# Kernel tuning notes

Hardware: AMD Instinct MI355X
Metric: run time of the kernel (lower is better)

## Reference

```python
import jax, jax.numpy as jnp
import numpy as np

DIM = 256
NUM_HEADS = 4
WINDOW = 64
EPS = 1e-6


def setup_inputs() -> dict:
    key = jax.random.key(0)
    ks = jax.random.split(key, 12)
    d = DIM
    s = 0.02
    return {
        "x": jax.random.normal(ks[0], (4, 2049, d), dtype=jnp.float32),
        "norm1_w": jnp.ones((d,), jnp.float32),
        "in_proj_w": jax.random.normal(ks[1], (3 * d, d), jnp.float32) * s,
        "in_proj_b": jnp.zeros((3 * d,), jnp.float32),
        "out_proj_w": jax.random.normal(ks[2], (d, d), jnp.float32) * s,
        "out_proj_b": jnp.zeros((d,), jnp.float32),
        "norm2_w": jnp.ones((d,), jnp.float32),
        "w1": jax.random.normal(ks[3], (2 * d, d), jnp.float32) * s,
        "b1": jnp.zeros((2 * d,), jnp.float32),
        "w2": jax.random.normal(ks[4], (d, 2 * d), jnp.float32) * s,
        "b2": jnp.zeros((d,), jnp.float32),
    }


def _rmsnorm(x, w):
    r = jax.lax.rsqrt(jnp.mean(x * x, axis=-1, keepdims=True) + EPS)
    return x * r * w


def _factorized_mask(size):
    # global token 0 attends/attended everywhere; others banded within WINDOW
    idx = jnp.arange(size)
    band = jnp.abs(idx[:, None] - idx[None, :]) <= WINDOW
    allowed = band | (idx[:, None] == 0) | (idx[None, :] == 0)
    return jnp.where(allowed, 0.0, -jnp.inf).astype(jnp.float32)


def reference(x, norm1_w, in_proj_w, in_proj_b, out_proj_w, out_proj_b,
              norm2_w, w1, b1, w2, b2):
    B, S, D = x.shape
    H = NUM_HEADS
    dh = D // H
    residual = x
    h = _rmsnorm(x, norm1_w)
    # fused qkv projection (torch MHA in_proj): [B,S,3D]
    qkv = h @ in_proj_w.T + in_proj_b
    q, k, v = jnp.split(qkv, 3, axis=-1)
    q = q.reshape(B, S, H, dh).transpose(0, 2, 1, 3)  # [B,H,S,dh]
    k = k.reshape(B, S, H, dh).transpose(0, 2, 1, 3)
    v = v.reshape(B, S, H, dh).transpose(0, 2, 1, 3)
    scores = jnp.einsum("bhqd,bhkd->bhqk", q, k) / jnp.sqrt(jnp.float32(dh))
    scores = scores + _factorized_mask(S)  # additive -inf mask
    attn = jax.nn.softmax(scores, axis=-1)
    ctx = jnp.einsum("bhqk,bhkd->bhqd", attn, v)
    ctx = ctx.transpose(0, 2, 1, 3).reshape(B, S, D)
    attn_out = ctx @ out_proj_w.T + out_proj_b
    x1 = residual + attn_out
    h2 = _rmsnorm(x1, norm2_w)
    ffn = jax.nn.gelu(h2 @ w1.T + b1, approximate=False) @ w2.T + b2
    return x1 + ffn
```

## Files before the change

kernel.cpp:

```cpp
#include <hip/hip_runtime.h>
#include <hip/hip_bf16.h>
#include <math.h>

#define BATCH 4
#define SEQ 2049
#define DIMD 256
#define WIN 64
#define M_ROWS (BATCH * SEQ)
#define M_PAD 8320

#define QT16 129
#define NKB 10
#define PSTR 168
#define CSTR 264
#define GSTR 136
#define VGUARD 64
#define VW 2256
#define QKSTR 512

#define NSPLIT 33
#define VT_F4 288768

typedef __attribute__((ext_vector_type(8))) short short8;
typedef __attribute__((ext_vector_type(4))) float f32x4;
typedef __hip_bfloat16 bf16;

__device__ __forceinline__ float b2f(short u) {
    union { unsigned int i; float f; } c;
    c.i = ((unsigned int)(unsigned short)u) << 16;
    return c.f;
}
__device__ __forceinline__ short f2b(float f) {
    bf16 h = __float2bfloat16(f);
    return *reinterpret_cast<short*>(&h);
}

__global__ __launch_bounds__(256) void prep_kernel(
        const float* __restrict__ wq, const float* __restrict__ wo,
        const float* __restrict__ w1, const float* __restrict__ w2,
        bf16* __restrict__ oq, bf16* __restrict__ oo,
        bf16* __restrict__ o1, bf16* __restrict__ o2,
        const float* __restrict__ x, const float* __restrict__ nw,
        bf16* __restrict__ h, float4* __restrict__ vTz) {
    const int bi = blockIdx.x, tid = threadIdx.x;
    if (bi < 2048) {
        int i = bi * 256 + tid;
        if (i < 196608)      oq[i]          = __float2bfloat16(wq[i]);
        else if (i < 262144) oo[i - 196608] = __float2bfloat16(wo[i - 196608]);
        else if (i < 393216) o1[i - 262144] = __float2bfloat16(w1[i - 262144]);
        else                 o2[i - 393216] = __float2bfloat16(w2[i - 393216]);
        return;
    }
    if (bi >= 4097) {
        int zi = (bi - 4097) * 256 + tid;
        #pragma unroll
        for (int it = 0; it < 3; it++) {
            int idx = zi + it * 512 * 256;
            if (idx < VT_F4) vTz[idx] = (float4){0.f, 0.f, 0.f, 0.f};
        }
        return;
    }
    int wid = tid >> 6, lane = tid & 63;
    int row = (bi - 2048) * 4 + wid;
    if (row >= M_ROWS) return;
    const float4 v = reinterpret_cast<const float4*>(x + (size_t)row * DIMD)[lane];
    float ss = v.x * v.x + v.y * v.y + v.z * v.z + v.w * v.w;
    #pragma unroll
    for (int o = 1; o < 64; o <<= 1) ss += __shfl_xor(ss, o, 64);
    float r = rsqrtf(ss * (1.0f / DIMD) + 1e-6f);
    const float4 wv = reinterpret_cast<const float4*>(nw)[lane];
    bf16* hp = h + (size_t)row * DIMD + lane * 4;
    hp[0] = __float2bfloat16(v.x * r * wv.x);
    hp[1] = __float2bfloat16(v.y * r * wv.y);
    hp[2] = __float2bfloat16(v.z * r * wv.z);
    hp[3] = __float2bfloat16(v.w * r * wv.w);
}

__global__ __launch_bounds__(256) void gemm_qkv(
        const bf16* __restrict__ A, const bf16* __restrict__ B,
        const float* __restrict__ bias, bf16* __restrict__ qk, short* __restrict__ vT) {
    __shared__ __align__(16) short lA[8 * 128 * 8];
    __shared__ __align__(16) short lB[8 * 128 * 8];
    const int tid = threadIdx.x, lane = tid & 63, wid = tid >> 6;
    const int m0 = blockIdx.x * 128;
    const int n0 = blockIdx.y * 128;
    const int wr = wid >> 1, wc = wid & 1;
    const int r = lane & 15, g = lane >> 4;
    const int K = 256;

    f32x4 acc[4][4];
    #pragma unroll
    for (int i = 0; i < 4; i++)
        #pragma unroll
        for (int j = 0; j < 4; j++) acc[i][j] = (f32x4){0.f, 0.f, 0.f, 0.f};

    for (int k0 = 0; k0 < K; k0 += 64) {
        #pragma unroll
        for (int it = 0; it < 4; ++it) {
            int c = it * 256 + tid;
            int kc = c >> 7, row = c & 127;
            __builtin_amdgcn_global_load_lds(
                (const __attribute__((address_space(1))) void*)(A + (size_t)(m0 + row) * K + k0 + kc * 8),
                (__attribute__((address_space(3))) void*)&lA[c * 8], 16, 0, 0);
        }
        #pragma unroll
        for (int it = 0; it < 4; ++it) {
            int c = it * 256 + tid;
            int kc = c >> 7, row = c & 127;
            __builtin_amdgcn_global_load_lds(
                (const __attribute__((address_space(1))) void*)(B + (size_t)(n0 + row) * K + k0 + kc * 8),
                (__attribute__((address_space(3))) void*)&lB[c * 8], 16, 0, 0);
        }
        __syncthreads();
        #pragma unroll
        for (int kk = 0; kk < 2; kk++) {
            short8 a[4], b[4];
            #pragma unroll
            for (int mi = 0; mi < 4; mi++)
                a[mi] = *reinterpret_cast<const short8*>(&lA[((kk * 4 + g) * 128 + wr * 64 + mi * 16 + r) * 8]);
            #pragma unroll
            for (int ni = 0; ni < 4; ni++)
                b[ni] = *reinterpret_cast<const short8*>(&lB[((kk * 4 + g) * 128 + wc * 64 + ni * 16 + r) * 8]);
            #pragma unroll
            for (int mi = 0; mi < 4; mi++)
                #pragma unroll
                for (int ni = 0; ni < 4; ni++)
                    acc[mi][ni] = __builtin_amdgcn_mfma_f32_16x16x32_bf16(a[mi], b[ni], acc[mi][ni], 0, 0, 0);
        }
        __syncthreads();
    }

    const int c0 = lane & 15, r0 = (lane >> 4) * 4;
    const bool isV = (n0 >= 512);
    #pragma unroll
    for (int mi = 0; mi < 4; mi++) {
        #pragma unroll
        for (int ni = 0; ni < 4; ni++) {
            int col = n0 + wc * 64 + ni * 16 + c0;
            float bv = bias[col];
            #pragma unroll
            for (int j = 0; j < 4; j++) {
                int row = m0 + wr * 64 + mi * 16 + r0 + j;
                if (row < M_ROWS) {
                    float v = acc[mi][ni][j] + bv;
                    if (!isV) {
                        qk[(size_t)row * QKSTR + col] = __float2bfloat16(v);
                    } else {
                        int dcol = col - 512, hh = dcol >> 6, d = dcol & 63;
                        int bb = row >> 11;
                        int js = row - bb * SEQ;
                        if (js < 0) { bb--; js += SEQ; }
                        vT[((size_t)((bb * 4 + hh) * 64 + d)) * VW + VGUARD + js] = f2b(v);
                    }
                }
            }
        }
    }
}

__global__ __launch_bounds__(256) void attn_partial(const bf16* __restrict__ qk,
                                                    const short* __restrict__ vT,
                                                    float* __restrict__ part) {
    __shared__ float q_s[64];
    __shared__ float p_s[64];
    __shared__ float meta[2];
    __shared__ float osum[4][64];
    const int tid = threadIdx.x;
    const int bh = blockIdx.x / NSPLIT, s = blockIdx.x % NSPLIT;
    const int b = bh >> 2, h = bh & 3;
    const size_t base = (size_t)b * SEQ;
    const int j0 = s * 64;
    const int lane = tid & 63, wid = tid >> 6;

    if (tid < 64) q_s[tid] = __bfloat162float(qk[base * QKSTR + h * 64 + tid]);
    __syncthreads();

    if (wid == 0) {
        int j = j0 + lane;
        float sc = -1e30f;
        if (j < SEQ) {
            const short8* kp = reinterpret_cast<const short8*>(
                reinterpret_cast<const short*>(qk) + (base + j) * QKSTR + 256 + h * 64);
            float acc = 0.f;
            #pragma unroll
            for (int d8 = 0; d8 < 8; ++d8) {
                short8 kv = kp[d8];
                #pragma unroll
                for (int e = 0; e < 8; ++e) acc += q_s[d8 * 8 + e] * b2f(kv[e]);
            }
            sc = acc * 0.125f;
        }
        float mx = sc;
        #pragma unroll
        for (int o = 1; o < 64; o <<= 1) mx = fmaxf(mx, __shfl_xor(mx, o, 64));
        float p = (j < SEQ) ? expf(sc - mx) : 0.f;
        p_s[lane] = p;
        float l = p;
        #pragma unroll
        for (int o = 1; o < 64; o <<= 1) l += __shfl_xor(l, o, 64);
        if (lane == 0) { meta[0] = mx; meta[1] = l; }
    }
    __syncthreads();

    const short* vrow = vT + ((size_t)bh * 64 + lane) * VW + VGUARD + j0;
    float oa = 0.f;
    #pragma unroll
    for (int i0 = 0; i0 < 16; i0++) {
        int i = wid + i0 * 4;
        if (j0 + i < SEQ) oa += p_s[i] * b2f(vrow[i]);
    }
    osum[wid][lane] = oa;
    __syncthreads();
    if (wid == 0) {
        float o = osum[0][lane] + osum[1][lane] + osum[2][lane] + osum[3][lane];
        float* pp = part + (size_t)(bh * NSPLIT + s) * 66;
        pp[lane] = o;
        if (lane == 0) { pp[64] = meta[0]; pp[65] = meta[1]; }
    }
}

__global__ __launch_bounds__(256) void attn_or(
        const bf16* __restrict__ qkb, const short* __restrict__ vT,
        const float* __restrict__ part, const bf16* __restrict__ wo,
        const float* __restrict__ ob, const float* __restrict__ x,
        const float* __restrict__ nw, float* __restrict__ x1, bf16* __restrict__ h2) {
    __shared__ short p_lds[4][16][PSTR];
    __shared__ short ctx_lds[16][CSTR];
    __shared__ float osq[4][16];
    const short* qk = reinterpret_cast<const short*>(qkb);
    const int tid = threadIdx.x, lane = tid & 63, h = tid >> 6;
    const int qt = blockIdx.x % QT16;
    const int b = blockIdx.x / QT16;
    const int bh = b * 4 + h;
    const size_t rbase = (size_t)b * SEQ;
    const int q0 = qt * 16;
    const int jbase = q0 - 64;
    const int lrow = lane & 15;
    const int koff = (lane >> 4) * 8;
    const int c0 = lrow, r0 = (lane >> 4) * 4;

    int qrow = q0 + lrow; if (qrow > SEQ - 1) qrow = SEQ - 1;
    const short* qp = qk + (rbase + qrow) * QKSTR + h * 64;
    short8 aq0 = *reinterpret_cast<const short8*>(qp + koff);
    short8 aq1 = *reinterpret_cast<const short8*>(qp + 32 + koff);

    const short* k0p = qk + rbase * QKSTR + 256 + h * 64;
    short8 k0a = *reinterpret_cast<const short8*>(k0p + koff);
    short8 k0b = *reinterpret_cast<const short8*>(k0p + 32 + koff);
    float s0 = 0.f;
    #pragma unroll
    for (int e = 0; e < 8; e++)
        s0 += b2f(aq0[e]) * b2f(k0a[e]) + b2f(aq1[e]) * b2f(k0b[e]);
    s0 += __shfl_xor(s0, 16, 64);
    s0 += __shfl_xor(s0, 32, 64);

    f32x4 s[NKB];
    #pragma unroll
    for (int n = 0; n < NKB; n++) {
        int j = jbase + n * 16 + lrow;
        int jc = j < 0 ? 0 : (j > SEQ - 1 ? SEQ - 1 : j);
        const short* kp = qk + (rbase + jc) * QKSTR + 256 + h * 64;
        short8 bk0 = *reinterpret_cast<const short8*>(kp + koff);
        short8 bk1 = *reinterpret_cast<const short8*>(kp + 32 + koff);
        f32x4 acc = (f32x4){0.f, 0.f, 0.f, 0.f};
        acc = __builtin_amdgcn_mfma_f32_16x16x32_bf16(aq0, bk0, acc, 0, 0, 0);
        acc = __builtin_amdgcn_mfma_f32_16x16x32_bf16(aq1, bk1, acc, 0, 0, 0);
        s[n] = acc;
    }

    const float SC = 0.125f * 1.44269504088896340736f;
    const bool g1 = (jbase > 0);
    float s0q[4], m4[4];
    #pragma unroll
    for (int jj = 0; jj < 4; jj++) {
        s0q[jj] = __shfl(s0, r0 + jj, 64) * SC;
        m4[jj] = g1 ? s0q[jj] : -1e30f;
    }
    #pragma unroll
    for (int n = 0; n < NKB; n++) {
        int j = jbase + n * 16 + c0;
        bool jv = (j >= 0) && (j < SEQ);
        #pragma unroll
        for (int jj = 0; jj < 4; jj++) {
            int q = q0 + r0 + jj;
            int dd = q - j; if (dd < 0) dd = -dd;
            bool allowed = jv && (dd <= WIN || j == 0);
            float v = allowed ? s[n][jj] * SC : -1e30f;
            s[n][jj] = v;
            m4[jj] = fmaxf(m4[jj], v);
        }
    }
    #pragma unroll
    for (int o = 1; o < 16; o <<= 1) {
        #pragma unroll
        for (int jj = 0; jj < 4; jj++) m4[jj] = fmaxf(m4[jj], __shfl_xor(m4[jj], o, 64));
    }

    float p0[4], l4[4];
    #pragma unroll
    for (int jj = 0; jj < 4; jj++) {
        p0[jj] = g1 ? exp2f(s0q[jj] - m4[jj]) : 0.f;
        l4[jj] = p0[jj];
    }
    #pragma unroll
    for (int n = 0; n < NKB; n++) {
        #pragma unroll
        for (int jj = 0; jj < 4; jj++) {
            float p = exp2f(s[n][jj] - m4[jj]);
            l4[jj] += p;
            p_lds[h][r0 + jj][n * 16 + c0] = f2b(p);
        }
    }
    #pragma unroll
    for (int o = 1; o < 16; o <<= 1) {
        #pragma unroll
        for (int jj = 0; jj < 4; jj++) l4[jj] += __shfl_xor(l4[jj], o, 64);
    }

    f32x4 o[4];
    #pragma unroll
    for (int dn = 0; dn < 4; dn++) o[dn] = (f32x4){0.f, 0.f, 0.f, 0.f};
    #pragma unroll
    for (int ks = 0; ks < NKB / 2; ks++) {
        short8 ap = *reinterpret_cast<const short8*>(&p_lds[h][lrow][ks * 32 + koff]);
        int cc = VGUARD + jbase + ks * 32 + koff;
        #pragma unroll
        for (int dn = 0; dn < 4; dn++) {
            short8 bv = *reinterpret_cast<const short8*>(
                vT + ((size_t)bh * 64 + dn * 16 + lrow) * VW + cc);
            o[dn] = __builtin_amdgcn_mfma_f32_16x16x32_bf16(ap, bv, o[dn], 0, 0, 0);
        }
    }

    #pragma unroll
    for (int jj = 0; jj < 4; jj++) {
        int q = q0 + r0 + jj;
        int ql = r0 + jj;
        float rl = 1.0f / l4[jj];
        #pragma unroll
        for (int dn = 0; dn < 4; dn++) {
            float v0 = b2f(vT[((size_t)bh * 64 + dn * 16 + c0) * VW + VGUARD]);
            float val = (o[dn][jj] + p0[jj] * v0) * rl;
            if (q >= 1) ctx_lds[ql][h * 64 + dn * 16 + c0] = f2b(val);
        }
    }

    if (qt == 0) {
        float m = (lane < NSPLIT) ? part[(size_t)(bh * NSPLIT + lane) * 66 + 64] : -1e30f;
        #pragma unroll
        for (int o2 = 1; o2 < 64; o2 <<= 1) m = fmaxf(m, __shfl_xor(m, o2, 64));
        float L = 0.f, ov = 0.f;
        for (int sp = 0; sp < NSPLIT; sp++) {
            const float* pp = part + (size_t)(bh * NSPLIT + sp) * 66;
            float w = expf(pp[64] - m);
            L += pp[65] * w;
            ov += pp[lane] * w;
        }
        ctx_lds[0][h * 64 + lane] = f2b(ov / L);
    }
    __syncthreads();

    f32x4 oacc[4];
    #pragma unroll
    for (int ni = 0; ni < 4; ni++) oacc[ni] = (f32x4){0.f, 0.f, 0.f, 0.f};
    #pragma unroll
    for (int ks = 0; ks < 8; ks++) {
        short8 a = *reinterpret_cast<const short8*>(&ctx_lds[lrow][ks * 32 + koff]);
        #pragma unroll
        for (int ni = 0; ni < 4; ni++) {
            short8 bfrag = *reinterpret_cast<const short8*>(
                reinterpret_cast<const short*>(wo) + (size_t)(h * 64 + ni * 16 + lrow) * 256 + ks * 32 + koff);
            oacc[ni] = __builtin_amdgcn_mfma_f32_16x16x32_bf16(a, bfrag, oacc[ni], 0, 0, 0);
        }
    }

    float ssq[4];
    #pragma unroll
    for (int jj = 0; jj < 4; jj++) {
        int row = q0 + r0 + jj;
        float sq = 0.f;
        if (row < SEQ) {
            #pragma unroll
            for (int ni = 0; ni < 4; ni++) {
                int col = h * 64 + ni * 16 + c0;
                float v = oacc[ni][jj] + ob[col] + x[(rbase + row) * 256 + col];
                oacc[ni][jj] = v;
                x1[(rbase + row) * 256 + col] = v;
                sq += v * v;
            }
        }
        ssq[jj] = sq;
    }
    #pragma unroll
    for (int o2 = 1; o2 < 16; o2 <<= 1) {
        #pragma unroll
        for (int jj = 0; jj < 4; jj++) ssq[jj] += __shfl_xor(ssq[jj], o2, 64);
    }
    if (c0 == 0) {
        #pragma unroll
        for (int jj = 0; jj < 4; jj++) osq[h][r0 + jj] = ssq[jj];
    }
    __syncthreads();
    #pragma unroll
    for (int jj = 0; jj < 4; jj++) {
        int lr = r0 + jj;
        int row = q0 + lr;
        if (row < SEQ) {
            float tot = osq[0][lr] + osq[1][lr] + osq[2][lr] + osq[3][lr];
            float rs = rsqrtf(tot * (1.0f / 256.0f) + 1e-6f);
            #pragma unroll
            for (int ni = 0; ni < 4; ni++) {
                int col = h * 64 + ni * 16 + c0;
                h2[(rbase + row) * 256 + col] = __float2bfloat16(oacc[ni][jj] * rs * nw[col]);
            }
        }
    }
}

__global__ __launch_bounds__(256) void ffn_fused(
        const bf16* __restrict__ h2, const bf16* __restrict__ w1b, const float* __restrict__ b1,
        const bf16* __restrict__ w2b, const float* __restrict__ b2, const float* __restrict__ x1,
        float* __restrict__ out) {
    __shared__ short g_lds[32][GSTR];
    const int tid = threadIdx.x, lane = tid & 63, wid = tid >> 6;
    const int m0 = blockIdx.x * 32;
    const int lrow = lane & 15;
    const int koff = (lane >> 4) * 8;
    const int c0 = lrow, r0 = (lane >> 4) * 4;

    f32x4 oacc[2][4];
    #pragma unroll
    for (int mi = 0; mi < 2; mi++)
        #pragma unroll
        for (int ni = 0; ni < 4; ni++) oacc[mi][ni] = (f32x4){0.f, 0.f, 0.f, 0.f};

    int ar[2];
    #pragma unroll
    for (int mi = 0; mi < 2; mi++) {
        int rr = m0 + mi * 16 + lrow;
        ar[mi] = rr < M_ROWS ? rr : M_ROWS - 1;
    }

    for (int ch = 0; ch < 4; ch++) {
        f32x4 gacc[2][2];
        #pragma unroll
        for (int mi = 0; mi < 2; mi++)
            #pragma unroll
            for (int ni = 0; ni < 2; ni++) gacc[mi][ni] = (f32x4){0.f, 0.f, 0.f, 0.f};
        #pragma unroll
        for (int ks = 0; ks < 8; ks++) {
            short8 a[2];
            #pragma unroll
            for (int mi = 0; mi < 2; mi++)
                a[mi] = *reinterpret_cast<const short8*>(
                    reinterpret_cast<const short*>(h2) + (size_t)ar[mi] * 256 + ks * 32 + koff);
            #pragma unroll
            for (int ni = 0; ni < 2; ni++) {
                short8 bfrag = *reinterpret_cast<const short8*>(
                    reinterpret_cast<const short*>(w1b) +
                    (size_t)(ch * 128 + wid * 32 + ni * 16 + lrow) * 256 + ks * 32 + koff);
                #pragma unroll
                for (int mi = 0; mi < 2; mi++)
                    gacc[mi][ni] = __builtin_amdgcn_mfma_f32_16x16x32_bf16(a[mi], bfrag, gacc[mi][ni], 0, 0, 0);
            }
        }
        if (ch > 0) __syncthreads();
        #pragma unroll
        for (int mi = 0; mi < 2; mi++) {
            #pragma unroll
            for (int ni = 0; ni < 2; ni++) {
                int colg = wid * 32 + ni * 16 + c0;
                float bv = b1[ch * 128 + colg];
                #pragma unroll
                for (int jj = 0; jj < 4; jj++) {
                    float v = gacc[mi][ni][jj] + bv;
                    v = 0.5f * v * (1.0f + erff(v * 0.70710678118654752f));
                    g_lds[mi * 16 + r0 + jj][colg] = f2b(v);
                }
            }
        }
        __syncthreads();
        #pragma unroll
        for (int k = 0; k < 4; k++) {
            short8 ag[2];
            #pragma unroll
            for (int mi = 0; mi < 2; mi++)
                ag[mi] = *reinterpret_cast<const short8*>(&g_lds[mi * 16 + lrow][k * 32 + koff]);
            #pragma unroll
            for (int ni = 0; ni < 4; ni++) {
                short8 bfrag = *reinterpret_cast<const short8*>(
                    reinterpret_cast<const short*>(w2b) +
                    (size_t)(wid * 64 + ni * 16 + lrow) * 512 + ch * 128 + k * 32 + koff);
                #pragma unroll
                for (int mi = 0; mi < 2; mi++)
                    oacc[mi][ni] = __builtin_amdgcn_mfma_f32_16x16x32_bf16(ag[mi], bfrag, oacc[mi][ni], 0, 0, 0);
            }
        }
    }

    #pragma unroll
    for (int mi = 0; mi < 2; mi++) {
        #pragma unroll
        for (int ni = 0; ni < 4; ni++) {
            int col = wid * 64 + ni * 16 + c0;
            float bv = b2[col];
            #pragma unroll
            for (int jj = 0; jj < 4; jj++) {
                int row = m0 + mi * 16 + r0 + jj;
                if (row < M_ROWS)
                    out[(size_t)row * 256 + col] = oacc[mi][ni][jj] + bv + x1[(size_t)row * 256 + col];
            }
        }
    }
}

extern "C" void kernel_launch(void* const* d_in, const int* in_sizes, int n_in,
                              void* d_out, int out_size, void* d_ws, size_t ws_size,
                              hipStream_t stream) {
    const float* x         = (const float*)d_in[0];
    const float* norm1_w   = (const float*)d_in[1];
    const float* in_proj_w = (const float*)d_in[2];
    const float* in_proj_b = (const float*)d_in[3];
    const float* out_proj_w= (const float*)d_in[4];
    const float* out_proj_b= (const float*)d_in[5];
    const float* norm2_w   = (const float*)d_in[6];
    const float* w1        = (const float*)d_in[7];
    const float* b1        = (const float*)d_in[8];
    const float* w2        = (const float*)d_in[9];
    const float* b2        = (const float*)d_in[10];
    float* out = (float*)d_out;

    char* ws = (char*)d_ws;
    size_t off = 0;
    auto take = [&](size_t bytes) {
        char* p = ws + off;
        off = (off + bytes + 255) & ~(size_t)255;
        return p;
    };
    bf16* h_bf   = (bf16*)take((size_t)M_PAD * 256 * 2);
    bf16* qk_bf  = (bf16*)take((size_t)M_PAD * QKSTR * 2);
    float* x1    = (float*)take((size_t)M_PAD * 256 * 4);
    bf16* h2_bf  = (bf16*)take((size_t)M_PAD * 256 * 2);
    bf16* wq_bf  = (bf16*)take(768 * 256 * 2);
    bf16* wo_bf  = (bf16*)take(256 * 256 * 2);
    bf16* w1_bf  = (bf16*)take(512 * 256 * 2);
    bf16* w2_bf  = (bf16*)take(256 * 512 * 2);
    float* part  = (float*)take((size_t)16 * NSPLIT * 66 * 4);
    short* vT    = (short*)take((size_t)16 * 64 * VW * 2);
    (void)ws_size; (void)in_sizes; (void)n_in; (void)out_size;

    prep_kernel<<<dim3(4609), dim3(256), 0, stream>>>(
        in_proj_w, out_proj_w, w1, w2, wq_bf, wo_bf, w1_bf, w2_bf,
        x, norm1_w, h_bf, (float4*)vT);
    gemm_qkv<<<dim3(65, 6), dim3(256), 0, stream>>>(h_bf, wq_bf, in_proj_b, qk_bf, vT);
    attn_partial<<<dim3(16 * NSPLIT), dim3(256), 0, stream>>>(qk_bf, vT, part);
    attn_or<<<dim3(4 * QT16), dim3(256), 0, stream>>>(
        qk_bf, vT, part, wo_bf, out_proj_b, x, norm2_w, x1, h2_bf);
    ffn_fused<<<dim3(257), dim3(256), 0, stream>>>(h2_bf, w1_bf, b1, w2_bf, b2, x1, out);
}
```

Baseline: 121.4 us.

## Split fused FFN into two LDS-tiled GEMMs with async global-to-LDS loads

Replaces the single fused FFN kernel, which read A and B fragments straight from global memory for 32-row tiles, with two launches of a templated 128-row tiled GEMM. The new GEMM stages tiles in LDS through global_load_lds, gaining reuse across waves. The GELU intermediate is now written to a bf16 workspace buffer in global memory and read back by the second GEMM. This adds an extra launch and intermediate traffic but aims for better operand reuse and more efficient MFMA feeding.

```diff
diff --git a/kernel.cpp b/kernel.cpp
--- a/kernel.cpp
+++ b/kernel.cpp
@@ -13,7 +13,6 @@
 #define NKB 10
 #define PSTR 168
 #define CSTR 264
-#define GSTR 136
 #define VGUARD 64
 #define VW 2256
 #define QKSTR 512
@@ -151,6 +150,87 @@
                         int js = row - bb * SEQ;
                         if (js < 0) { bb--; js += SEQ; }
                         vT[((size_t)((bb * 4 + hh) * 64 + d)) * VW + VGUARD + js] = f2b(v);
+                    }
+                }
+            }
+        }
+    }
+}
+
+template<int MODE, int BN>
+__global__ __launch_bounds__(256) void gemm_lds(
+        const bf16* __restrict__ A, const bf16* __restrict__ B,
+        const float* __restrict__ bias, const float* __restrict__ resid,
+        void* __restrict__ C, int M, int N, int K) {
+    constexpr int FN = BN / 32;
+    __shared__ __align__(16) short lA[8 * 128 * 8];
+    __shared__ __align__(16) short lB[8 * BN * 8];
+    const int tid = threadIdx.x, lane = tid & 63, wid = tid >> 6;
+    const int m0 = blockIdx.x * 128;
+    const int n0 = blockIdx.y * BN;
+    const int wr = wid >> 1, wc = wid & 1;
+    const int r = lane & 15, g = lane >> 4;
+
+    f32x4 acc[4][FN];
+    #pragma unroll
+    for (int i = 0; i < 4; i++)
+        #pragma unroll
+        for (int j = 0; j < FN; j++) acc[i][j] = (f32x4){0.f, 0.f, 0.f, 0.f};
+
+    for (int k0 = 0; k0 < K; k0 += 64) {
+        #pragma unroll
+        for (int it = 0; it < 4; ++it) {
+            int c = it * 256 + tid;
+            int kc = c >> 7, row = c & 127;
+            __builtin_amdgcn_global_load_lds(
+                (const __attribute__((address_space(1))) void*)(A + (size_t)(m0 + row) * K + k0 + kc * 8),
+                (__attribute__((address_space(3))) void*)&lA[c * 8], 16, 0, 0);
+        }
+        #pragma unroll
+        for (int it = 0; it < BN / 32; ++it) {
+            int c = it * 256 + tid;
+            int kc = c / BN, row = c % BN;
+            __builtin_amdgcn_global_load_lds(
+                (const __attribute__((address_space(1))) void*)(B + (size_t)(n0 + row) * K + k0 + kc * 8),
+                (__attribute__((address_space(3))) void*)&lB[c * 8], 16, 0, 0);
+        }
+        __syncthreads();
+        #pragma unroll
+        for (int kk = 0; kk < 2; kk++) {
+            short8 a[4], b[FN];
+            #pragma unroll
+            for (int mi = 0; mi < 4; mi++)
+                a[mi] = *reinterpret_cast<const short8*>(&lA[((kk * 4 + g) * 128 + wr * 64 + mi * 16 + r) * 8]);
+            #pragma unroll
+            for (int ni = 0; ni < FN; ni++)
+                b[ni] = *reinterpret_cast<const short8*>(&lB[((kk * 4 + g) * BN + wc * (BN / 2) + ni * 16 + r) * 8]);
+            #pragma unroll
+            for (int mi = 0; mi < 4; mi++)
+                #pragma unroll
+                for (int ni = 0; ni < FN; ni++)
+                    acc[mi][ni] = __builtin_amdgcn_mfma_f32_16x16x32_bf16(a[mi], b[ni], acc[mi][ni], 0, 0, 0);
+        }
+        __syncthreads();
+    }
+
+    const int c0 = lane & 15, r0 = (lane >> 4) * 4;
+    #pragma unroll
+    for (int mi = 0; mi < 4; mi++) {
+        #pragma unroll
+        for (int ni = 0; ni < FN; ni++) {
+            int col = n0 + wc * (BN / 2) + ni * 16 + c0;
+            float bv = bias[col];
+            #pragma unroll
+            for (int j = 0; j < 4; j++) {
+                int row = m0 + wr * 64 + mi * 16 + r0 + j;
+                if (row < M) {
+                    float v = acc[mi][ni][j] + bv;
+                    if (MODE == 2) v = 0.5f * v * (1.0f + erff(v * 0.70710678118654752f));
+                    if (MODE == 1) {
+                        v += resid[(size_t)row * N + col];
+                        reinterpret_cast<float*>(C)[(size_t)row * N + col] = v;
+                    } else {
+                        reinterpret_cast<bf16*>(C)[(size_t)row * N + col] = __float2bfloat16(v);
                     }
                 }
             }
@@ -417,103 +497,6 @@
     }
 }
 
-__global__ __launch_bounds__(256) void ffn_fused(
-        const bf16* __restrict__ h2, const bf16* __restrict__ w1b, const float* __restrict__ b1,
-        const bf16* __restrict__ w2b, const float* __restrict__ b2, const float* __restrict__ x1,
-        float* __restrict__ out) {
-    __shared__ short g_lds[32][GSTR];
-    const int tid = threadIdx.x, lane = tid & 63, wid = tid >> 6;
-    const int m0 = blockIdx.x * 32;
-    const int lrow = lane & 15;
-    const int koff = (lane >> 4) * 8;
-    const int c0 = lrow, r0 = (lane >> 4) * 4;
-
-    f32x4 oacc[2][4];
-    #pragma unroll
-    for (int mi = 0; mi < 2; mi++)
-        #pragma unroll
-        for (int ni = 0; ni < 4; ni++) oacc[mi][ni] = (f32x4){0.f, 0.f, 0.f, 0.f};
-
-    int ar[2];
-    #pragma unroll
-    for (int mi = 0; mi < 2; mi++) {
-        int rr = m0 + mi * 16 + lrow;
-        ar[mi] = rr < M_ROWS ? rr : M_ROWS - 1;
-    }
-
-    for (int ch = 0; ch < 4; ch++) {
-        f32x4 gacc[2][2];
-        #pragma unroll
-        for (int mi = 0; mi < 2; mi++)
-            #pragma unroll
-            for (int ni = 0; ni < 2; ni++) gacc[mi][ni] = (f32x4){0.f, 0.f, 0.f, 0.f};
-        #pragma unroll
-        for (int ks = 0; ks < 8; ks++) {
-            short8 a[2];
-            #pragma unroll
-            for (int mi = 0; mi < 2; mi++)
-                a[mi] = *reinterpret_cast<const short8*>(
-                    reinterpret_cast<const short*>(h2) + (size_t)ar[mi] * 256 + ks * 32 + koff);
-            #pragma unroll
-            for (int ni = 0; ni < 2; ni++) {
-                short8 bfrag = *reinterpret_cast<const short8*>(
-                    reinterpret_cast<const short*>(w1b) +
-                    (size_t)(ch * 128 + wid * 32 + ni * 16 + lrow) * 256 + ks * 32 + koff);
-                #pragma unroll
-                for (int mi = 0; mi < 2; mi++)
-                    gacc[mi][ni] = __builtin_amdgcn_mfma_f32_16x16x32_bf16(a[mi], bfrag, gacc[mi][ni], 0, 0, 0);
-            }
-        }
-        if (ch > 0) __syncthreads();
-        #pragma unroll
-        for (int mi = 0; mi < 2; mi++) {
-            #pragma unroll
-            for (int ni = 0; ni < 2; ni++) {
-                int colg = wid * 32 + ni * 16 + c0;
-                float bv = b1[ch * 128 + colg];
-                #pragma unroll
-                for (int jj = 0; jj < 4; jj++) {
-                    float v = gacc[mi][ni][jj] + bv;
-                    v = 0.5f * v * (1.0f + erff(v * 0.70710678118654752f));
-                    g_lds[mi * 16 + r0 + jj][colg] = f2b(v);
-                }
-            }
-        }
-        __syncthreads();
-        #pragma unroll
-        for (int k = 0; k < 4; k++) {
-            short8 ag[2];
-            #pragma unroll
-            for (int mi = 0; mi < 2; mi++)
-                ag[mi] = *reinterpret_cast<const short8*>(&g_lds[mi * 16 + lrow][k * 32 + koff]);
-            #pragma unroll
-            for (int ni = 0; ni < 4; ni++) {
-                short8 bfrag = *reinterpret_cast<const short8*>(
-                    reinterpret_cast<const short*>(w2b) +
-                    (size_t)(wid * 64 + ni * 16 + lrow) * 512 + ch * 128 + k * 32 + koff);
-                #pragma unroll
-                for (int mi = 0; mi < 2; mi++)
-                    oacc[mi][ni] = __builtin_amdgcn_mfma_f32_16x16x32_bf16(ag[mi], bfrag, oacc[mi][ni], 0, 0, 0);
-            }
-        }
-    }
-
-    #pragma unroll
-    for (int mi = 0; mi < 2; mi++) {
-        #pragma unroll
-        for (int ni = 0; ni < 4; ni++) {
-            int col = wid * 64 + ni * 16 + c0;
-            float bv = b2[col];
-            #pragma unroll
-            for (int jj = 0; jj < 4; jj++) {
-                int row = m0 + mi * 16 + r0 + jj;
-                if (row < M_ROWS)
-                    out[(size_t)row * 256 + col] = oacc[mi][ni][jj] + bv + x1[(size_t)row * 256 + col];
-            }
-        }
-    }
-}
-
 extern "C" void kernel_launch(void* const* d_in, const int* in_sizes, int n_in,
                               void* d_out, int out_size, void* d_ws, size_t ws_size,
                               hipStream_t stream) {
@@ -530,6 +513,7 @@
     const float* b2        = (const float*)d_in[10];
     float* out = (float*)d_out;
 
+    const int M = M_ROWS;
     char* ws = (char*)d_ws;
     size_t off = 0;
     auto take = [&](size_t bytes) {
@@ -541,6 +525,7 @@
     bf16* qk_bf  = (bf16*)take((size_t)M_PAD * QKSTR * 2);
     float* x1    = (float*)take((size_t)M_PAD * 256 * 4);
     bf16* h2_bf  = (bf16*)take((size_t)M_PAD * 256 * 2);
+    bf16* g_bf   = (bf16*)take((size_t)M_PAD * 512 * 2);
     bf16* wq_bf  = (bf16*)take(768 * 256 * 2);
     bf16* wo_bf  = (bf16*)take(256 * 256 * 2);
     bf16* w1_bf  = (bf16*)take(512 * 256 * 2);
@@ -556,5 +541,8 @@
     attn_partial<<<dim3(16 * NSPLIT), dim3(256), 0, stream>>>(qk_bf, vT, part);
     attn_or<<<dim3(4 * QT16), dim3(256), 0, stream>>>(
         qk_bf, vT, part, wo_bf, out_proj_b, x, norm2_w, x1, h2_bf);
-    ffn_fused<<<dim3(257), dim3(256), 0, stream>>>(h2_bf, w1_bf, b1, w2_bf, b2, x1, out);
-}
+    gemm_lds<2, 128><<<dim3(65, 4), dim3(256), 0, stream>>>(h2_bf, w1_bf, b1, (const float*)nullptr,
+                                                            (void*)g_bf, M, 512, 256);
+    gemm_lds<1, 64><<<dim3(65, 4), dim3(256), 0, stream>>>(g_bf, w2_bf, b2, x1,
+                                                           (void*)out, M, 256, 512);
+}
```

New measurement: 124.0 us. 2.1% more time.
